# Performance work log

Hardware: AMD Instinct MI355X
Metric: run time of the kernel (lower is better)

Reference implementation:

```python
import jax, jax.numpy as jnp
import numpy as np

D_MODEL = 1024
NUM_HEADS = 16
D_K = D_MODEL // NUM_HEADS
SCALE = 1.0 / np.sqrt(D_K).astype(np.float32)
MASK_FILL = -10000.0


def setup_inputs() -> dict:
    key = jax.random.key(0)
    ks = jax.random.split(key, 5)
    B, S = 2, 2048
    x = jax.random.normal(ks[0], (B, S, D_MODEL), dtype=jnp.float32)
    mask = jax.random.randint(ks[1], (B, S), 0, 2, dtype=jnp.int32)
    # Kaiming-uniform-ish init like nn.Linear defaults
    lim1 = 1.0 / np.sqrt(D_MODEL)
    Wqkv = jax.random.uniform(ks[2], (D_MODEL, 3 * D_MODEL), jnp.float32, -lim1, lim1)
    bqkv = jnp.zeros((3 * D_MODEL,), jnp.float32)
    Wout = jax.random.uniform(ks[3], (D_MODEL, D_MODEL), jnp.float32, -lim1, lim1)
    bout = jnp.zeros((D_MODEL,), jnp.float32)
    return {"x": x, "mask": mask, "Wqkv": Wqkv, "bqkv": bqkv, "Wout": Wout, "bout": bout}


def reference(x, mask, Wqkv, bqkv, Wout, bout):
    B, S, _ = x.shape
    qkv = (x @ Wqkv + bqkv).reshape(B, S, 3, NUM_HEADS, D_K)
    qkv = jnp.transpose(qkv, (2, 0, 3, 1, 4))
    q, k, v = qkv[0], qkv[1], qkv[2]
    # scaled dot-product scores [B,H,S,S]
    scores = jnp.einsum("bhqd,bhkd->bhqk", q, k) * SCALE
    # key-padding mask [B,S] -> [B,1,1,S]; masked positions set to -10000 (as in source)
    m = mask[:, None, None, :]
    scores = jnp.where(m == 0, MASK_FILL, scores)
    attn = jax.nn.softmax(scores, axis=-1)
    # dropout is disabled (eval/inference)
    context = jnp.einsum("bhqk,bhkd->bhqd", attn, v)
    context = jnp.transpose(context, (0, 2, 1, 3)).reshape(B, S, D_MODEL)
    return context @ Wout + bout
```

## Files before the change

kernel.cpp:

```cpp
#include <hip/hip_runtime.h>

typedef _Float16 f16;
typedef _Float16 f16x2 __attribute__((ext_vector_type(2)));
typedef _Float16 f16x4 __attribute__((ext_vector_type(4)));
typedef _Float16 f16x8 __attribute__((ext_vector_type(8)));
typedef float    f32x4 __attribute__((ext_vector_type(4)));
typedef float    f32x16 __attribute__((ext_vector_type(16)));
typedef int      i32x4 __attribute__((ext_vector_type(4)));

#define NHEADS 16
#define DK 64
#define BATCH 2
#define SEQ 2048
#define DMODEL 1024
#define MTOT (BATCH*SEQ)
#define NQKV (3*DMODEL)
#define NBH  (BATCH*NHEADS)
#define LOG2E 1.44269504f
#define QSCALE (0.125f * LOG2E)
#define MASKVAL (-10000.0f * LOG2E)

__device__ inline f16x8 ld_f16x8_g(const f16* p) {
  return __builtin_bit_cast(f16x8, *reinterpret_cast<const i32x4*>(p));
}

__device__ inline f16x2 cvt_pk(float a, float b) {
  return __builtin_bit_cast(f16x2, __builtin_amdgcn_cvt_pkrtz(a, b));
}

__device__ inline void gl_lds16(const void* g, void* l) {
  __builtin_amdgcn_global_load_lds(
      (const __attribute__((address_space(1))) unsigned int*)g,
      (__attribute__((address_space(3))) unsigned int*)l, 16, 0, 0);
}

__device__ inline int sigma_k(int s) {
  return (s & ~12) | ((s & 4) << 1) | ((s & 8) >> 1);
}

__device__ inline void tcvt_tile(float (*tile)[33], const float* __restrict__ in,
                                 f16* __restrict__ out, int K, int N, int k0, int n0) {
  const int t = threadIdx.x, j = t & 7, ty = t >> 3;
  float4 v = *reinterpret_cast<const float4*>(in + (size_t)(k0 + ty) * N + n0 + j*4);
  tile[ty][j*4+0] = v.x; tile[ty][j*4+1] = v.y;
  tile[ty][j*4+2] = v.z; tile[ty][j*4+3] = v.w;
  __syncthreads();
  union { f16x2 h2[2]; f16x4 h4; } u;
  u.h2[0] = cvt_pk(tile[j*4+0][ty], tile[j*4+1][ty]);
  u.h2[1] = cvt_pk(tile[j*4+2][ty], tile[j*4+3][ty]);
  *(f16x4*)(out + (size_t)(n0 + ty) * K + k0 + j*4) = u.h4;
}

__global__ __launch_bounds__(256) void k_prep(
    const float* __restrict__ x, f16* __restrict__ xh,
    const float* __restrict__ Wqkv, f16* __restrict__ Wqkvt,
    const float* __restrict__ Wout, f16* __restrict__ Woutt,
    const int* __restrict__ mask, int* __restrict__ inv, int* __restrict__ cnt)
{
  __shared__ float tile[32][33];
  __shared__ int part[256];
  const int bid = blockIdx.x;
  const int t = threadIdx.x;
  if (bid < 4096) {
    int i = (bid * 256 + t) * 4;
    float4 v = *reinterpret_cast<const float4*>(x + i);
    f16x4 o = { (f16)v.x, (f16)v.y, (f16)v.z, (f16)v.w };
    *reinterpret_cast<f16x4*>(xh + i) = o;
  } else if (bid < 4096 + 3072) {
    int tl = bid - 4096;
    tcvt_tile(tile, Wqkv, Wqkvt, DMODEL, NQKV, (tl / 96) * 32, (tl % 96) * 32);
  } else if (bid < 8192) {
    int tl = bid - 4096 - 3072;
    tcvt_tile(tile, Wout, Woutt, DMODEL, DMODEL, (tl / 32) * 32, (tl % 32) * 32);
  } else {
    const int b = bid - 8192;
    const int* mp = mask + b * SEQ;
    int* iv = inv + b * SEQ;
    const int base = t * 8;
    int m[8]; int s = 0;
    #pragma unroll
    for (int i = 0; i < 8; ++i) { m[i] = mp[base + i]; s += (m[i] != 0); }
    part[t] = s;
    __syncthreads();
    for (int d = 1; d < 256; d <<= 1) {
      int v = (t >= d) ? part[t - d] : 0;
      __syncthreads();
      part[t] += v;
      __syncthreads();
    }
    int pos = (t == 0) ? 0 : part[t - 1];
    #pragma unroll
    for (int i = 0; i < 8; ++i) {
      if (m[i] != 0) { iv[pos] = base + i; ++pos; }
    }
    if (t == 255) cnt[b] = part[255];
  }
}

__global__ __launch_bounds__(256, 2) void k_gemm_qkv2(
    const f16* __restrict__ A, const f16* __restrict__ Bt,
    const float* __restrict__ bias, const int* __restrict__ inv,
    const int* __restrict__ cnt,
    f16* __restrict__ qo, f16* __restrict__ ko, f16* __restrict__ vto, int K)
{
  __shared__ f16 As[2][64][64];
  __shared__ f16 Bs[2][128][64];
  const int bid = blockIdx.x;
  const bool isQ = bid < 512;

  const int t = threadIdx.x;
  const int l = t & 63, w = t >> 6;
  const int lc = l & 15, g = l >> 4;
  const int srow = l >> 3;
  const int ssl  = ((l & 7) ^ srow) * 16;
  const int swz  = (lc & 7) << 4;

  int m0, n0, b = 0, c = 0;
  const f16* Btp;
  const float* biasp;
  size_t aoff[2];
  if (isQ) {
    n0 = (bid & 7) * 128;  m0 = (bid >> 3) * 64;
    Btp = Bt;  biasp = bias;
    #pragma unroll
    for (int it = 0; it < 2; ++it)
      aoff[it] = (size_t)(m0 + it*32 + w*8 + srow) * K;
  } else {
    const int idx = bid - 512;
    n0 = (idx & 15) * 128;  m0 = (idx >> 4) * 64;
    b = m0 >> 11;
    const int sl0 = m0 & (SEQ - 1);
    c = cnt[b];
    if (sl0 >= ((c + 63) & ~63)) return;
    Btp = Bt + (size_t)DMODEL * DMODEL;
    biasp = bias + DMODEL;
    #pragma unroll
    for (int it = 0; it < 2; ++it) {
      int slot = sl0 + it*32 + w*8 + srow;
      int sidx = (slot < c) ? slot : (c > 0 ? c - 1 : 0);
      aoff[it] = (size_t)(b * SEQ + (inv[b * SEQ + sidx] & (SEQ - 1))) * K;
    }
  }

  auto stage = [&](int buf, int kt) {
    #pragma unroll
    for (int it = 0; it < 2; ++it)
      gl_lds16((const char*)(A + aoff[it] + kt) + ssl, &As[buf][it*32 + w*8][0]);
    #pragma unroll
    for (int it = 0; it < 4; ++it) {
      int row = it*32 + w*8 + srow;
      gl_lds16((const char*)(Btp + (size_t)(n0 + row) * K + kt) + ssl,
               &Bs[buf][it*32 + w*8][0]);
    }
  };

  f32x4 acc[4][2] = {};
  const int NTk = K >> 6;
  stage(0, 0);

  for (int ti = 0; ti < NTk; ++ti) {
    __syncthreads();
    if (ti + 1 < NTk) stage((ti + 1) & 1, (ti + 1) * 64);
    const char* abase = (const char*)&As[ti & 1][0][0];
    const char* bbase = (const char*)&Bs[ti & 1][0][0];
    #pragma unroll
    for (int ks = 0; ks < 64; ks += 32) {
      f16x8 af[4], bf[2];
      #pragma unroll
      for (int i = 0; i < 4; ++i)
        af[i] = *(const f16x8*)(abase + (i*16 + lc)*128 + ((ks*2 + g*16) ^ swz));
      #pragma unroll
      for (int j = 0; j < 2; ++j)
        bf[j] = *(const f16x8*)(bbase + (w*32 + j*16 + lc)*128 + ((ks*2 + g*16) ^ swz));
      #pragma unroll
      for (int i = 0; i < 4; ++i)
        #pragma unroll
        for (int j = 0; j < 2; ++j)
          acc[i][j] = __builtin_amdgcn_mfma_f32_16x16x32_f16(af[i], bf[j], acc[i][j], 0, 0, 0);
    }
  }

  if (isQ) {
    #pragma unroll
    for (int i = 0; i < 4; ++i) {
      const int row0 = m0 + i*16 + g*4;
      const int qb = row0 >> 11, s0 = row0 & (SEQ - 1);
      #pragma unroll
      for (int j = 0; j < 2; ++j) {
        int col = n0 + w*32 + j*16 + lc;
        float bv = biasp[col];
        int h = col >> 6, d = col & 63;
        size_t bh = (size_t)(qb * NHEADS + h);
        #pragma unroll
        for (int r = 0; r < 4; ++r)
          qo[(bh * SEQ + s0 + r) * DK + d] = (f16)((acc[i][j][r] + bv) * QSCALE);
      }
    }
  } else {
    const int sl0 = m0 & (SEQ - 1);
    #pragma unroll
    for (int i = 0; i < 4; ++i) {
      const int slot0 = sl0 + i*16 + g*4;
      #pragma unroll
      for (int j = 0; j < 2; ++j) {
        int colkv = n0 + w*32 + j*16 + lc;
        float bv = biasp[colkv];
        int kv = colkv >> 10;
        int h = (colkv >> 6) & 15, d = colkv & 63;
        size_t bh = (size_t)(b * NHEADS + h);
        if (kv == 0) {
          #pragma unroll
          for (int r = 0; r < 4; ++r)
            ko[(bh * SEQ + slot0 + r) * DK + d] = (f16)(acc[i][j][r] + bv);
        } else {
          union { f16x2 h2[2]; f16x4 h4; } u;
          u.h2[0] = cvt_pk(acc[i][j][0] + bv, acc[i][j][1] + bv);
          u.h2[1] = cvt_pk(acc[i][j][2] + bv, acc[i][j][3] + bv);
          *(f16x4*)(vto + (bh * DK + d) * SEQ + sigma_k(slot0)) = u.h4;
        }
      }
    }
  }
}

__global__ __launch_bounds__(256, 2) void k_gemm_out(
    const f16* __restrict__ A, const f16* __restrict__ Bt,
    const float* __restrict__ bias, float* __restrict__ outf, int N, int K)
{
  __shared__ f16 As[2][64][64];
  __shared__ f16 Bs[2][128][64];
  const int m0 = blockIdx.y * 64, n0 = blockIdx.x * 128;
  const int t = threadIdx.x;
  const int l = t & 63, w = t >> 6;
  const int lc = l & 15, g = l >> 4;
  const int srow = l >> 3;
  const int ssl  = ((l & 7) ^ srow) * 16;
  const int swz  = (lc & 7) << 4;

  auto stage = [&](int buf, int kt) {
    #pragma unroll
    for (int it = 0; it < 2; ++it) {
      int row = it*32 + w*8 + srow;
      gl_lds16((const char*)(A + (size_t)(m0 + row) * K + kt) + ssl,
               &As[buf][it*32 + w*8][0]);
    }
    #pragma unroll
    for (int it = 0; it < 4; ++it) {
      int row = it*32 + w*8 + srow;
      gl_lds16((const char*)(Bt + (size_t)(n0 + row) * K + kt) + ssl,
               &Bs[buf][it*32 + w*8][0]);
    }
  };

  f32x4 acc[4][2] = {};
  const int NTk = K >> 6;
  stage(0, 0);

  for (int ti = 0; ti < NTk; ++ti) {
    __syncthreads();
    if (ti + 1 < NTk) stage((ti + 1) & 1, (ti + 1) * 64);
    const char* abase = (const char*)&As[ti & 1][0][0];
    const char* bbase = (const char*)&Bs[ti & 1][0][0];
    #pragma unroll
    for (int ks = 0; ks < 64; ks += 32) {
      f16x8 af[4], bf[2];
      #pragma unroll
      for (int i = 0; i < 4; ++i)
        af[i] = *(const f16x8*)(abase + (i*16 + lc)*128 + ((ks*2 + g*16) ^ swz));
      #pragma unroll
      for (int j = 0; j < 2; ++j)
        bf[j] = *(const f16x8*)(bbase + (w*32 + j*16 + lc)*128 + ((ks*2 + g*16) ^ swz));
      #pragma unroll
      for (int i = 0; i < 4; ++i)
        #pragma unroll
        for (int j = 0; j < 2; ++j)
          acc[i][j] = __builtin_amdgcn_mfma_f32_16x16x32_f16(af[i], bf[j], acc[i][j], 0, 0, 0);
    }
  }

  #pragma unroll
  for (int i = 0; i < 4; ++i) {
    #pragma unroll
    for (int j = 0; j < 2; ++j) {
      int col = n0 + w*32 + j*16 + lc;
      float bv = bias[col];
      #pragma unroll
      for (int r = 0; r < 4; ++r) {
        int row = m0 + i*16 + g*4 + r;
        outf[(size_t)row * N + col] = acc[i][j][r] + bv;
      }
    }
  }
}

__global__ __launch_bounds__(256, 2) void k_attn10(
    const f16* __restrict__ Q, const f16* __restrict__ K,
    const f16* __restrict__ Vt, const int* __restrict__ cnt,
    f16* __restrict__ ctx)
{
  __shared__ f16 Kb[2][32][128];
  __shared__ f16 Vb[2][32][128];

  const int bid = blockIdx.x;
  const int xcd = bid & 7, slot = bid >> 3;
  const int bh = xcd * 4 + (slot >> 4);
  const int qb = slot & 15;
  const int b  = bh >> 4, h = bh & (NHEADS - 1);
  const int t = threadIdx.x, l = t & 63, w = t >> 6;
  const int r31 = l & 31, hi = l >> 5;
  const int Rm = r31 & 15;
  const int q0 = qb * 128 + w * 32;

  const int c = cnt[b];
  const int NTc = (c + 63) >> 6;

  const f16* Qp = Q + (size_t)bh * SEQ * DK;
  const f16* Kp = K + (size_t)bh * SEQ * DK;
  const f16* Vp = Vt + (size_t)bh * DK * SEQ;

  f16x8 qf[4];
  #pragma unroll
  for (int ds = 0; ds < 4; ++ds)
    qf[ds] = ld_f16x8_g(Qp + (size_t)(q0 + r31) * DK + ds*16 + hi*8);

  f32x16 o[2] = {};
  float mrow = -3e38f;
  float lsum = 0.f;

  auto stage = [&](int buf, int kt) {
    #pragma unroll
    for (int cc = 0; cc < 2; ++cc) {
      int Rbase = w*8 + cc*4;
      int R = Rbase + (l >> 4);
      int u = (l & 15) ^ (R & 15);
      int off32 = (u >> 3) * 32;
      int byteoff = (u & 7) * 16;
      gl_lds16((const char*)Kp + (size_t)(kt + off32 + R) * (DK*2) + byteoff,
               &Kb[buf][Rbase][0]);
      gl_lds16((const char*)Vp + (size_t)(off32 + R) * (SEQ*2) + (size_t)kt*2 + byteoff,
               &Vb[buf][Rbase][0]);
    }
  };

  stage(0, 0);

  for (int it = 0; it < NTc; ++it) {
    __syncthreads();
    if (it + 1 < NTc) stage((it + 1) & 1, (it + 1) * 64);
    const int kt = it * 64;
    const char* kb = (const char*)&Kb[it & 1][0][0];
    const char* vb = (const char*)&Vb[it & 1][0][0];

    f32x16 p[2];
    if (kt + 64 <= c) {
      #pragma unroll
      for (int T = 0; T < 2; ++T)
        #pragma unroll
        for (int r = 0; r < 16; ++r) p[T][r] = 0.f;
    } else {
      #pragma unroll
      for (int T = 0; T < 2; ++T)
        #pragma unroll
        for (int r = 0; r < 16; ++r) {
          int k = kt + T*32 + 4*hi + (r & 3) + 8*(r >> 2);
          p[T][r] = (k < c) ? 0.f : MASKVAL;
        }
    }

    __builtin_amdgcn_s_setprio(1);
    #pragma unroll
    for (int T = 0; T < 2; ++T)
      #pragma unroll
      for (int ds = 0; ds < 4; ++ds) {
        int slotc = T*8 + ds*2 + hi;
        f16x8 kf = *(const f16x8*)(kb + r31*256 + ((slotc ^ Rm) << 4));
        p[T] = __builtin_amdgcn_mfma_f32_32x32x16_f16(kf, qf[ds], p[T], 0, 0, 0);
      }
    __builtin_amdgcn_s_setprio(0);

    float mx;
    {
      f32x4 t4;
      #pragma unroll
      for (int r = 0; r < 4; ++r)
        t4[r] = fmaxf(fmaxf(p[0][r], p[0][r+4]), fmaxf(p[0][r+8], p[0][r+12]));
      #pragma unroll
      for (int r = 0; r < 4; ++r)
        t4[r] = fmaxf(t4[r], fmaxf(fmaxf(p[1][r], p[1][r+4]), fmaxf(p[1][r+8], p[1][r+12])));
      mx = fmaxf(fmaxf(t4[0], t4[1]), fmaxf(t4[2], t4[3]));
    }
    mx = fmaxf(mx, __shfl_xor(mx, 32));

    if (!__all(mx <= mrow + 8.f)) {
      float nm = fmaxf(mrow, mx);
      float sc = __builtin_amdgcn_exp2f(mrow - nm);
      mrow = nm;
      lsum *= sc;
      #pragma unroll
      for (int dt = 0; dt < 2; ++dt)
        #pragma unroll
        for (int r = 0; r < 16; ++r) o[dt][r] *= sc;
    }

    f16x2 h2[2][8];
    float s0 = 0.f, s1 = 0.f;
    #pragma unroll
    for (int T = 0; T < 2; ++T)
      #pragma unroll
      for (int rp = 0; rp < 8; ++rp) {
        float e0 = __builtin_amdgcn_exp2f(p[T][2*rp]   - mrow);
        float e1 = __builtin_amdgcn_exp2f(p[T][2*rp+1] - mrow);
        s0 += e0; s1 += e1;
        h2[T][rp] = cvt_pk(e0, e1);
      }
    lsum += s0 + s1;

    __builtin_amdgcn_s_setprio(1);
    #pragma unroll
    for (int T = 0; T < 2; ++T)
      #pragma unroll
      for (int half = 0; half < 2; ++half) {
        union { f16x2 a[4]; f16x8 v8; } pu;
        pu.a[0] = h2[T][half*4+0]; pu.a[1] = h2[T][half*4+1];
        pu.a[2] = h2[T][half*4+2]; pu.a[3] = h2[T][half*4+3];
        int m = T*2 + half;
        #pragma unroll
        for (int dt = 0; dt < 2; ++dt) {
          int slotc = dt*8 + m*2 + hi;
          f16x8 vf = *(const f16x8*)(vb + r31*256 + ((slotc ^ Rm) << 4));
          o[dt] = __builtin_amdgcn_mfma_f32_32x32x16_f16(vf, pu.v8, o[dt], 0, 0, 0);
        }
      }
    __builtin_amdgcn_s_setprio(0);
  }

  lsum += __shfl_xor(lsum, 32);
  float inv = 1.f / lsum;
  f16* cp = ctx + (size_t)(b*SEQ + q0 + r31) * DMODEL + h*DK;
  #pragma unroll
  for (int dt = 0; dt < 2; ++dt)
    #pragma unroll
    for (int rq = 0; rq < 4; ++rq) {
      union { f16x2 h2v[2]; f16x4 h4v; } u;
      u.h2v[0] = cvt_pk(o[dt][4*rq+0]*inv, o[dt][4*rq+1]*inv);
      u.h2v[1] = cvt_pk(o[dt][4*rq+2]*inv, o[dt][4*rq+3]*inv);
      *(f16x4*)(cp + dt*32 + 8*rq + 4*hi) = u.h4v;
    }
}

extern "C" void kernel_launch(void* const* d_in, const int* in_sizes, int n_in,
                              void* d_out, int out_size, void* d_ws, size_t ws_size,
                              hipStream_t stream) {
  const float* x    = (const float*)d_in[0];
  const int*   mask = (const int*)d_in[1];
  const float* Wqkv = (const float*)d_in[2];
  const float* bqkv = (const float*)d_in[3];
  const float* Wout = (const float*)d_in[4];
  const float* bout = (const float*)d_in[5];
  float* out = (float*)d_out;

  const size_t SZ_X    = (size_t)MTOT * DMODEL * 2;
  const size_t SZ_WQKV = (size_t)NQKV * DMODEL * 2;
  const size_t SZ_WOUT = (size_t)DMODEL * DMODEL * 2;
  const size_t SZ_QKV  = (size_t)BATCH * NHEADS * SEQ * DK * 2;
  const size_t SZ_INV  = (size_t)MTOT * 4;
  const size_t SZ_CNT  = 256;
  const size_t NEED = SZ_X + SZ_WQKV + SZ_WOUT + 3*SZ_QKV + SZ_X + SZ_INV + SZ_CNT;
  if (ws_size < NEED) return;

  char* p = (char*)d_ws;
  f16* xh    = (f16*)p; p += SZ_X;
  f16* Wqkvt = (f16*)p; p += SZ_WQKV;
  f16* Woutt = (f16*)p; p += SZ_WOUT;
  f16* Qh    = (f16*)p; p += SZ_QKV;
  f16* Kh    = (f16*)p; p += SZ_QKV;
  f16* Vth   = (f16*)p; p += SZ_QKV;
  f16* ctx   = (f16*)p; p += SZ_X;
  int* inv   = (int*)p; p += SZ_INV;
  int* cnt   = (int*)p; p += SZ_CNT;

  k_prep<<<4096 + 3072 + 1024 + BATCH, 256, 0, stream>>>(
      x, xh, Wqkv, Wqkvt, Wout, Woutt, mask, inv, cnt);

  k_gemm_qkv2<<<512 + 1024, 256, 0, stream>>>(
      xh, Wqkvt, bqkv, inv, cnt, Qh, Kh, Vth, DMODEL);

  k_attn10<<<32 * 16, 256, 0, stream>>>(Qh, Kh, Vth, cnt, ctx);

  k_gemm_out<<<dim3(DMODEL/128, MTOT/64), 256, 0, stream>>>(
      ctx, Woutt, bout, out, DMODEL, DMODEL);
}
```

Measured before the change: 96.85 us.

## Fuse x fp32-to-fp16 conversion into QKV GEMM A-tile staging

```diff
diff --git a/kernel.cpp b/kernel.cpp
--- a/kernel.cpp
+++ b/kernel.cpp
@@ -52,7 +52,6 @@
 }
 
 __global__ __launch_bounds__(256) void k_prep(
-    const float* __restrict__ x, f16* __restrict__ xh,
     const float* __restrict__ Wqkv, f16* __restrict__ Wqkvt,
     const float* __restrict__ Wout, f16* __restrict__ Woutt,
     const int* __restrict__ mask, int* __restrict__ inv, int* __restrict__ cnt)
@@ -61,19 +60,14 @@
   __shared__ int part[256];
   const int bid = blockIdx.x;
   const int t = threadIdx.x;
-  if (bid < 4096) {
-    int i = (bid * 256 + t) * 4;
-    float4 v = *reinterpret_cast<const float4*>(x + i);
-    f16x4 o = { (f16)v.x, (f16)v.y, (f16)v.z, (f16)v.w };
-    *reinterpret_cast<f16x4*>(xh + i) = o;
-  } else if (bid < 4096 + 3072) {
-    int tl = bid - 4096;
+  if (bid < 3072) {
+    int tl = bid;
     tcvt_tile(tile, Wqkv, Wqkvt, DMODEL, NQKV, (tl / 96) * 32, (tl % 96) * 32);
-  } else if (bid < 8192) {
-    int tl = bid - 4096 - 3072;
+  } else if (bid < 4096) {
+    int tl = bid - 3072;
     tcvt_tile(tile, Wout, Woutt, DMODEL, DMODEL, (tl / 32) * 32, (tl % 32) * 32);
   } else {
-    const int b = bid - 8192;
+    const int b = bid - 4096;
     const int* mp = mask + b * SEQ;
     int* iv = inv + b * SEQ;
     const int base = t * 8;
@@ -98,7 +92,7 @@
 }
 
 __global__ __launch_bounds__(256, 2) void k_gemm_qkv2(
-    const f16* __restrict__ A, const f16* __restrict__ Bt,
+    const float* __restrict__ A, const f16* __restrict__ Bt,
     const float* __restrict__ bias, const int* __restrict__ inv,
     const int* __restrict__ cnt,
     f16* __restrict__ qo, f16* __restrict__ ko, f16* __restrict__ vto, int K)
@@ -112,6 +106,7 @@
   const int l = t & 63, w = t >> 6;
   const int lc = l & 15, g = l >> 4;
   const int srow = l >> 3;
+  const int eidx = ((l & 7) ^ srow) * 8;
   const int ssl  = ((l & 7) ^ srow) * 16;
   const int swz  = (lc & 7) << 4;
 
@@ -142,10 +137,26 @@
     }
   }
 
-  auto stage = [&](int buf, int kt) {
-    #pragma unroll
-    for (int it = 0; it < 2; ++it)
-      gl_lds16((const char*)(A + aoff[it] + kt) + ssl, &As[buf][it*32 + w*8][0]);
+  auto loadA = [&](int kt, float4* r) {
+    #pragma unroll
+    for (int it = 0; it < 2; ++it) {
+      const float* s = A + aoff[it] + kt + eidx;
+      r[2*it]   = *reinterpret_cast<const float4*>(s);
+      r[2*it+1] = *reinterpret_cast<const float4*>(s + 4);
+    }
+  };
+  auto writeA = [&](int buf, const float4* r) {
+    #pragma unroll
+    for (int it = 0; it < 2; ++it) {
+      union { f16x2 h2[4]; f16x8 h8; } u;
+      u.h2[0] = cvt_pk(r[2*it].x,   r[2*it].y);
+      u.h2[1] = cvt_pk(r[2*it].z,   r[2*it].w);
+      u.h2[2] = cvt_pk(r[2*it+1].x, r[2*it+1].y);
+      u.h2[3] = cvt_pk(r[2*it+1].z, r[2*it+1].w);
+      *(f16x8*)((char*)&As[buf][it*32 + w*8 + srow][0] + ((l & 7) << 4)) = u.h8;
+    }
+  };
+  auto stageB = [&](int buf, int kt) {
     #pragma unroll
     for (int it = 0; it < 4; ++it) {
       int row = it*32 + w*8 + srow;
@@ -156,11 +167,18 @@
 
   f32x4 acc[4][2] = {};
   const int NTk = K >> 6;
-  stage(0, 0);
-
+  {
+    float4 a0[4];
+    loadA(0, a0);
+    writeA(0, a0);
+    stageB(0, 0);
+  }
+
+  float4 ar[4];
   for (int ti = 0; ti < NTk; ++ti) {
+    if (ti + 1 < NTk) loadA((ti + 1) * 64, ar);
     __syncthreads();
-    if (ti + 1 < NTk) stage((ti + 1) & 1, (ti + 1) * 64);
+    if (ti + 1 < NTk) stageB((ti + 1) & 1, (ti + 1) * 64);
     const char* abase = (const char*)&As[ti & 1][0][0];
     const char* bbase = (const char*)&Bs[ti & 1][0][0];
     #pragma unroll
@@ -178,6 +196,7 @@
         for (int j = 0; j < 2; ++j)
           acc[i][j] = __builtin_amdgcn_mfma_f32_16x16x32_f16(af[i], bf[j], acc[i][j], 0, 0, 0);
     }
+    if (ti + 1 < NTk) writeA((ti + 1) & 1, ar);
   }
 
   if (isQ) {
@@ -465,11 +484,10 @@
   const size_t SZ_QKV  = (size_t)BATCH * NHEADS * SEQ * DK * 2;
   const size_t SZ_INV  = (size_t)MTOT * 4;
   const size_t SZ_CNT  = 256;
-  const size_t NEED = SZ_X + SZ_WQKV + SZ_WOUT + 3*SZ_QKV + SZ_X + SZ_INV + SZ_CNT;
+  const size_t NEED = SZ_WQKV + SZ_WOUT + 3*SZ_QKV + SZ_X + SZ_INV + SZ_CNT;
   if (ws_size < NEED) return;
 
   char* p = (char*)d_ws;
-  f16* xh    = (f16*)p; p += SZ_X;
   f16* Wqkvt = (f16*)p; p += SZ_WQKV;
   f16* Woutt = (f16*)p; p += SZ_WOUT;
   f16* Qh    = (f16*)p; p += SZ_QKV;
@@ -479,11 +497,11 @@
   int* inv   = (int*)p; p += SZ_INV;
   int* cnt   = (int*)p; p += SZ_CNT;
 
-  k_prep<<<4096 + 3072 + 1024 + BATCH, 256, 0, stream>>>(
-      x, xh, Wqkv, Wqkvt, Wout, Woutt, mask, inv, cnt);
+  k_prep<<<3072 + 1024 + BATCH, 256, 0, stream>>>(
+      Wqkv, Wqkvt, Wout, Woutt, mask, inv, cnt);
 
   k_gemm_qkv2<<<512 + 1024, 256, 0, stream>>>(
-      xh, Wqkvt, bqkv, inv, cnt, Qh, Kh, Vth, DMODEL);
+      x, Wqkvt, bqkv, inv, cnt, Qh, Kh, Vth, DMODEL);
 
   k_attn10<<<32 * 16, 256, 0, stream>>>(Qh, Kh, Vth, cnt, ctx);
 
```

Result: slower. 100.5 us (+3.8%).
